# Performance work log

Measured on AMD Instinct MI355X. Metric: run time of the kernel, lower is better.

## Reference

```python
import jax, jax.numpy as jnp
import numpy as np

B, E, H, NH, HD = 8, 1536, 256, 8, 32
L, V, NL, FF = 50, 50257, 4, 2048
BOS = 50256
EPS = 1e-5


def setup_inputs():
    key = jax.random.key(0)
    ks = jax.random.split(key, 12)
    s = 0.02

    def rn(k, shape):
        return jax.random.normal(k, shape, jnp.float32) * s

    return {
        "embedding": jax.random.normal(ks[0], (B, E), jnp.float32),
        "w_proj": rn(ks[1], (H, E)), "b_proj": jnp.zeros((H,), jnp.float32),
        "tok_emb": rn(ks[2], (V, H)),
        "pos_enc": rn(ks[3], (1, L, H)),
        "sa_in_w": rn(ks[4], (NL, 3 * H, H)), "sa_in_b": jnp.zeros((NL, 3 * H), jnp.float32),
        "sa_out_w": rn(ks[5], (NL, H, H)), "sa_out_b": jnp.zeros((NL, H), jnp.float32),
        "ca_in_w": rn(ks[6], (NL, 3 * H, H)), "ca_in_b": jnp.zeros((NL, 3 * H), jnp.float32),
        "ca_out_w": rn(ks[7], (NL, H, H)), "ca_out_b": jnp.zeros((NL, H), jnp.float32),
        "ff1_w": rn(ks[8], (NL, FF, H)), "ff1_b": jnp.zeros((NL, FF), jnp.float32),
        "ff2_w": rn(ks[9], (NL, H, FF)), "ff2_b": jnp.zeros((NL, H), jnp.float32),
        "ln_g": jnp.ones((NL, 3, H), jnp.float32), "ln_b": jnp.zeros((NL, 3, H), jnp.float32),
        "fc_w": rn(ks[10], (V, H)), "fc_b": jnp.zeros((V,), jnp.float32),
    }


def _ln(x, g, b):
    m = jnp.mean(x, -1, keepdims=True)
    v = jnp.mean((x - m) ** 2, -1, keepdims=True)
    return (x - m) * jax.lax.rsqrt(v + EPS) * g + b


def _mha(q_in, kv_in, in_w, in_b, out_w, out_b, mask):
    wq, wk, wv = jnp.split(in_w, 3, axis=0)
    bq, bk, bv = jnp.split(in_b, 3)

    def heads(t):
        b_, l_, _ = t.shape
        return t.reshape(b_, l_, NH, HD).transpose(0, 2, 1, 3)  # [B,NH,L,HD]

    q = heads(q_in @ wq.T + bq)
    k = heads(kv_in @ wk.T + bk)
    v = heads(kv_in @ wv.T + bv)
    scores = jnp.einsum('bhqd,bhkd->bhqk', q, k) * (1.0 / np.sqrt(HD))
    if mask is not None:
        scores = scores + mask
    a = jax.nn.softmax(scores, axis=-1)
    o = jnp.einsum('bhqk,bhkd->bhqd', a, v)
    o = o.transpose(0, 2, 1, 3).reshape(q_in.shape)
    return o @ out_w.T + out_b


def _decoder(x, mem, mask, p):
    # nn.TransformerDecoderLayer, post-LN, relu FFN
    for l in range(NL):
        x = _ln(x + _mha(x, x, p['sa_in_w'][l], p['sa_in_b'][l], p['sa_out_w'][l], p['sa_out_b'][l], mask), p['ln_g'][l, 0], p['ln_b'][l, 0])
        x = _ln(x + _mha(x, mem, p['ca_in_w'][l], p['ca_in_b'][l], p['ca_out_w'][l], p['ca_out_b'][l], None), p['ln_g'][l, 1], p['ln_b'][l, 1])
        h = jax.nn.relu(x @ p['ff1_w'][l].T + p['ff1_b'][l]) @ p['ff2_w'][l].T + p['ff2_b'][l]
        x = _ln(x + h, p['ln_g'][l, 2], p['ln_b'][l, 2])
    return x


def _forward(embedding, tok_emb, pos_enc, w_proj, b_proj, fc_w, fc_b, p):
    mem = (embedding @ w_proj.T + b_proj)[:, None, :]  # [B,1,H] single-token memory
    causal = jnp.tril(jnp.ones((L, L), bool))
    mask = jnp.where(causal, 0.0, -jnp.inf)[None, None]  # [1,1,L,L]
    tokens0 = jnp.full((B, L), BOS, jnp.int32)  # padded token buffer; pos 0 = BOS

    # At step t the original recomputes the decoder over the first t+1 tokens and
    # reads the last position. With a causal mask, position t of a full-length
    # decode depends only on tokens[:t+1], so decoding the padded buffer and
    # slicing position t is exactly the same math (no-KV-cache recompute kept).
    def step(tokens, t):
        x = tok_emb[tokens] + pos_enc[:, :L]
        x = _decoder(x, mem, mask, p)
        h_t = jax.lax.dynamic_slice_in_dim(x, t, 1, axis=1)[:, 0]  # [B,H]
        logits = h_t @ fc_w.T + fc_b  # [B,V]
        nxt = jnp.argmax(logits, -1).astype(jnp.int32)
        tokens = jax.lax.dynamic_update_slice_in_dim(tokens, nxt[:, None], t + 1, axis=1)
        return tokens, logits

    _, logits = jax.lax.scan(step, tokens0, jnp.arange(L - 1))
    return jnp.transpose(logits, (1, 0, 2))  # [B, L-1, V]


def reference(embedding, w_proj, b_proj, tok_emb, pos_enc, sa_in_w, sa_in_b, sa_out_w, sa_out_b, ca_in_w, ca_in_b, ca_out_w, ca_out_b, ff1_w, ff1_b, ff2_w, ff2_b, ln_g, ln_b, fc_w, fc_b):
    p = dict(sa_in_w=sa_in_w, sa_in_b=sa_in_b, sa_out_w=sa_out_w, sa_out_b=sa_out_b,
             ca_in_w=ca_in_w, ca_in_b=ca_in_b, ca_out_w=ca_out_w, ca_out_b=ca_out_b,
             ff1_w=ff1_w, ff1_b=ff1_b, ff2_w=ff2_w, ff2_b=ff2_b, ln_g=ln_g, ln_b=ln_b)
    return _forward(embedding, tok_emb, pos_enc, w_proj, b_proj, fc_w, fc_b, p)
```

## Files before the change

### kernel.cpp

```cpp
#include <hip/hip_runtime.h>

#define NV 50257
#define BOSTOK 50256
#define LNEPS 1e-5f
#define NSTEP 49
#define NBLK 256
#define RPB 197
#define DYN_LDS_BYTES ((256 * 52 + 50 * 256) * 4)
#define FSTR 64

#define FQKV(l)   (0 + (l))
#define FU(l)     (4 + (l))
#define FFPX(l,j) (8 + (l) * 8 + (j))
#define FFC(j)    (48 + (j))
#define FMEMF     56
#define FCAF      57

#define WS4_MEM 4096
#define WS4_CA  6144
#define WS4_XF  14336
#define WS4_Q   16384
#define WS4_K   18432
#define WS4_V   20480
#define WS4_U   22528
#define WS4_FFP 30720
#define WS4_PV  63488
#define WS4_PI  65536

__device__ __forceinline__ float gld(const float* p) {
  return __hip_atomic_load(const_cast<float*>(p), __ATOMIC_RELAXED, __HIP_MEMORY_SCOPE_AGENT);
}
__device__ __forceinline__ void gst(float* p, float v) {
  __hip_atomic_store(p, v, __ATOMIC_RELAXED, __HIP_MEMORY_SCOPE_AGENT);
}
__device__ __forceinline__ void gsti(int* p, int v) {
  __hip_atomic_store(p, v, __ATOMIC_RELAXED, __HIP_MEMORY_SCOPE_AGENT);
}
__device__ __forceinline__ unsigned fld(unsigned* p) {
  return __hip_atomic_load(p, __ATOMIC_RELAXED, __HIP_MEMORY_SCOPE_AGENT);
}
__device__ __forceinline__ void spin_burst(float z) {
#pragma unroll
  for (int i = 0; i < 64; ++i) z = __builtin_fmaf(z, 1.0000001f, 1e-30f);
  asm volatile("" :: "v"(z));
}
__device__ __forceinline__ void bump(unsigned* f) {
  asm volatile("s_waitcnt vmcnt(0)" ::: "memory");
  __syncthreads();
  if (threadIdx.x == 0)
    __hip_atomic_fetch_add(f, 1u, __ATOMIC_RELAXED, __HIP_MEMORY_SCOPE_AGENT);
}
__device__ __forceinline__ void bump8(unsigned* f) {
  asm volatile("s_waitcnt vmcnt(0)" ::: "memory");
  __syncthreads();
  if (threadIdx.x == 0)
    for (int j = 0; j < 8; ++j)
      __hip_atomic_fetch_add(f + j * FSTR, 1u, __ATOMIC_RELAXED, __HIP_MEMORY_SCOPE_AGENT);
}
__device__ __forceinline__ unsigned waitf(unsigned* f, unsigned tgt, unsigned* sh) {
  if (threadIdx.x == 0) {
    unsigned v = fld(f);
    while (v < tgt) { spin_burst((float)v); v = fld(f); }
    *sh = v;
  }
  __syncthreads();
  return *sh;
}
__device__ __forceinline__ unsigned wait_fcsum(unsigned* FL, unsigned tgt, unsigned* sh) {
  if (threadIdx.x == 0) {
    const unsigned* bp = FL + 48 * FSTR;
    unsigned s;
    for (;;) {
      unsigned a0, a1, a2, a3, a4, a5, a6, a7;
      asm volatile(
          "global_load_dword %0, %8, off sc0 sc1\n\t"
          "global_load_dword %1, %8, off offset:256 sc0 sc1\n\t"
          "global_load_dword %2, %8, off offset:512 sc0 sc1\n\t"
          "global_load_dword %3, %8, off offset:768 sc0 sc1\n\t"
          "global_load_dword %4, %8, off offset:1024 sc0 sc1\n\t"
          "global_load_dword %5, %8, off offset:1280 sc0 sc1\n\t"
          "global_load_dword %6, %8, off offset:1536 sc0 sc1\n\t"
          "global_load_dword %7, %8, off offset:1792 sc0 sc1\n\t"
          "s_waitcnt vmcnt(0)"
          : "=&v"(a0), "=&v"(a1), "=&v"(a2), "=&v"(a3),
            "=&v"(a4), "=&v"(a5), "=&v"(a6), "=&v"(a7)
          : "v"(bp) : "memory");
      s = a0 + a1 + a2 + a3 + a4 + a5 + a6 + a7;
      if (s >= tgt) break;
      spin_burst((float)s);
    }
    *sh = s;
  }
  __syncthreads();
  return *sh;
}

__device__ __forceinline__ void pull2p(float* x, float* y,
    const float* p0, const float* p1, unsigned salt) {
  asm("global_load_dword %0, %2, off sc0 sc1\n\t"
      "global_load_dword %1, %3, off sc0 sc1\n\t"
      "s_waitcnt vmcnt(0)"
      : "=&v"(*x), "=&v"(*y)
      : "v"(p0), "v"(p1), "v"(salt));
}
__device__ __forceinline__ void pull3p(float* x, float* y, float* z,
    const float* p0, const float* p1, const float* p2, unsigned salt) {
  asm("global_load_dword %0, %3, off sc0 sc1\n\t"
      "global_load_dword %1, %4, off sc0 sc1\n\t"
      "global_load_dword %2, %5, off sc0 sc1\n\t"
      "s_waitcnt vmcnt(0)"
      : "=&v"(*x), "=&v"(*y), "=&v"(*z)
      : "v"(p0), "v"(p1), "v"(p2), "v"(salt));
}
__device__ __forceinline__ void pull8p(float r[8],
    const float* p0, const float* p1, const float* p2, const float* p3,
    const float* p4, const float* p5, const float* p6, const float* p7, unsigned salt) {
  float a0, a1, a2, a3, a4, a5, a6, a7;
  asm("global_load_dword %0, %8, off sc0 sc1\n\t"
      "global_load_dword %1, %9, off sc0 sc1\n\t"
      "global_load_dword %2, %10, off sc0 sc1\n\t"
      "global_load_dword %3, %11, off sc0 sc1\n\t"
      "global_load_dword %4, %12, off sc0 sc1\n\t"
      "global_load_dword %5, %13, off sc0 sc1\n\t"
      "global_load_dword %6, %14, off sc0 sc1\n\t"
      "global_load_dword %7, %15, off sc0 sc1\n\t"
      "s_waitcnt vmcnt(0)"
      : "=&v"(a0), "=&v"(a1), "=&v"(a2), "=&v"(a3),
        "=&v"(a4), "=&v"(a5), "=&v"(a6), "=&v"(a7)
      : "v"(p0), "v"(p1), "v"(p2), "v"(p3), "v"(p4), "v"(p5), "v"(p6), "v"(p7), "v"(salt));
  r[0] = a0; r[1] = a1; r[2] = a2; r[3] = a3;
  r[4] = a4; r[5] = a5; r[6] = a6; r[7] = a7;
}
__device__ __forceinline__ void pull1_2q(float* u, float4* f0, float4* f1,
    const float* pu, const float* pf, unsigned salt) {
  asm("global_load_dword %0, %3, off sc0 sc1\n\t"
      "global_load_dwordx4 %1, %4, off sc0 sc1\n\t"
      "global_load_dwordx4 %2, %4, off offset:16 sc0 sc1\n\t"
      "s_waitcnt vmcnt(0)"
      : "=&v"(*u), "=&v"(*f0), "=&v"(*f1)
      : "v"(pu), "v"(pf), "v"(salt));
}
__device__ __forceinline__ void pull4x8(float4 r[8],
    const float* p0, const float* p1, const float* p2, const float* p3, unsigned salt) {
  float4 a0, a1, a2, a3, a4, a5, a6, a7;
  asm("global_load_dwordx4 %0, %8, off sc0 sc1\n\t"
      "global_load_dwordx4 %1, %8, off offset:16 sc0 sc1\n\t"
      "global_load_dwordx4 %2, %9, off sc0 sc1\n\t"
      "global_load_dwordx4 %3, %9, off offset:16 sc0 sc1\n\t"
      "global_load_dwordx4 %4, %10, off sc0 sc1\n\t"
      "global_load_dwordx4 %5, %10, off offset:16 sc0 sc1\n\t"
      "global_load_dwordx4 %6, %11, off sc0 sc1\n\t"
      "global_load_dwordx4 %7, %11, off offset:16 sc0 sc1\n\t"
      "s_waitcnt vmcnt(0)"
      : "=&v"(a0), "=&v"(a1), "=&v"(a2), "=&v"(a3),
        "=&v"(a4), "=&v"(a5), "=&v"(a6), "=&v"(a7)
      : "v"(p0), "v"(p1), "v"(p2), "v"(p3), "v"(salt));
  r[0] = a0; r[1] = a1; r[2] = a2; r[3] = a3;
  r[4] = a4; r[5] = a5; r[6] = a6; r[7] = a7;
}

__device__ __forceinline__ float block_ln256(float v, int tid, float* red8, float g, float bta) {
  float s = v, s2 = v * v;
#pragma unroll
  for (int m = 32; m >= 1; m >>= 1) { s += __shfl_xor(s, m); s2 += __shfl_xor(s2, m); }
  int w = tid >> 6;
  __syncthreads();
  if ((tid & 63) == 0) { red8[w] = s; red8[4 + w] = s2; }
  __syncthreads();
  s = red8[0] + red8[1] + red8[2] + red8[3];
  s2 = red8[4] + red8[5] + red8[6] + red8[7];
  float mn = s * (1.0f / 256.0f);
  float var = s2 * (1.0f / 256.0f) - mn * mn;
  float rs = rsqrtf(var + LNEPS);
  return (v - mn) * rs * g + bta;
}

__device__ __forceinline__ void finalln_fc(int bid, int tid, int t, unsigned salt,
                                           const float* u, const float* ffp,
                                           const float* ff2_b, const float* ln_g,
                                           const float* ln_b,
                                           const float* fc_w, const float* fc_b, float* out,
                                           float* pv, int* pi,
                                           float* xl, float* rv, int* ri, float* red8) {
  {
    float u8[8];
    pull8p(u8, u + 3 * 2048 + 0 * 256 + tid, u + 3 * 2048 + 1 * 256 + tid,
           u + 3 * 2048 + 2 * 256 + tid, u + 3 * 2048 + 3 * 256 + tid,
           u + 3 * 2048 + 4 * 256 + tid, u + 3 * 2048 + 5 * 256 + tid,
           u + 3 * 2048 + 6 * 256 + tid, u + 3 * 2048 + 7 * 256 + tid, salt);
    float4 fA[8], fB[8];
    const float* fb = ffp + 1 * 16384;
    pull4x8(fA, fb + (0 * 256 + tid) * 8, fb + (1 * 256 + tid) * 8,
            fb + (2 * 256 + tid) * 8, fb + (3 * 256 + tid) * 8, salt);
    pull4x8(fB, fb + (4 * 256 + tid) * 8, fb + (5 * 256 + tid) * 8,
            fb + (6 * 256 + tid) * 8, fb + (7 * 256 + tid) * 8, salt);
    float g = ln_g[(3 * 3 + 2) * 256 + tid], bt = ln_b[(3 * 3 + 2) * 256 + tid];
    float f2b = ff2_b[3 * 256 + tid];
#pragma unroll
    for (int b = 0; b < 8; ++b) {
      float4 q0 = (b < 4) ? fA[2 * b] : fB[2 * (b - 4)];
      float4 q1 = (b < 4) ? fA[2 * b + 1] : fB[2 * (b - 4) + 1];
      float a = u8[b] + f2b + q0.x + q0.y + q0.z + q0.w + q1.x + q1.y + q1.z + q1.w;
      xl[b * 260 + tid] = block_ln256(a, tid, red8, g, bt);
    }
  }
  __syncthreads();
  int r = tid >> 3, b = tid & 7;
  float bv = -3e38f; int bi = 2147483647;
  int base = bid * RPB;
  for (int i = 0; i < 7; ++i) {
    int rr = i * 32 + r, row = base + rr;
    if (rr < RPB && row < NV) {
      float acc = fc_b[row];
      const float4* w4 = reinterpret_cast<const float4*>(fc_w + (size_t)row * 256);
      const float4* xv = reinterpret_cast<const float4*>(xl + b * 260);
      for (int k = 0; k < 64; ++k) {
        float4 wv = w4[k]; float4 xq = xv[k];
        acc += wv.x * xq.x + wv.y * xq.y + wv.z * xq.z + wv.w * xq.w;
      }
      out[(size_t)(b * 49 + t) * NV + row] = acc;
      if (acc > bv || (acc == bv && row < bi)) { bv = acc; bi = row; }
    }
  }
  rv[tid] = bv; ri[tid] = bi;
  __syncthreads();
  for (int off = 128; off >= 8; off >>= 1) {
    if (tid < off) {
      float v = rv[tid + off]; int id = ri[tid + off];
      if (v > rv[tid] || (v == rv[tid] && id < ri[tid])) { rv[tid] = v; ri[tid] = id; }
    }
    __syncthreads();
  }
  if (tid < 8) { gst(pv + bid * 8 + tid, rv[tid]); gsti(pi + bid * 8 + tid, ri[tid]); }
}

__global__ __launch_bounds__(256) void k_flow6(
    const float* __restrict__ emb, const float* __restrict__ w_proj, const float* __restrict__ b_proj,
    const float* __restrict__ tok_emb, const float* __restrict__ pos_enc,
    const float* __restrict__ sa_in_w, const float* __restrict__ sa_in_b,
    const float* __restrict__ sa_out_w, const float* __restrict__ sa_out_b,
    const float* __restrict__ ca_in_w, const float* __restrict__ ca_in_b,
    const float* __restrict__ ca_out_w, const float* __restrict__ ca_out_b,
    const float* __restrict__ ff1_w, const float* __restrict__ ff1_b,
    const float* __restrict__ ff2_w, const float* __restrict__ ff2_b,
    const float* __restrict__ ln_g, const float* __restrict__ ln_b,
    const float* __restrict__ fc_w, const float* __restrict__ fc_b,
    float* __restrict__ out, float* __restrict__ wsf, int* __restrict__ wsi) {
  extern __shared__ float dynlds[];
  const int bid = blockIdx.x, tid = threadIdx.x;

  unsigned* FL = (unsigned*)wsf;
  float* mem = wsf + WS4_MEM;
  float* ca  = wsf + WS4_CA;
  float* qb  = wsf + WS4_Q;
  float* kb  = wsf + WS4_K;
  float* vb  = wsf + WS4_V;
  float* u   = wsf + WS4_U;
  float* ffp = wsf + WS4_FFP;
  float* pv  = wsf + WS4_PV;
  int*   pi  = wsi + WS4_PI;

  __shared__ float xl[8 * 260];
  __shared__ float h1l[256 * 9];
  __shared__ float ql[256], ol[256], ph[8 * 64];
  __shared__ float red8[8];
  __shared__ float rv[256];
  __shared__ int   ri[256];
  __shared__ int   toks[8];
  __shared__ unsigned saltsh;
  __shared__ float el[1536];

  if (bid < 64) {
    int b = bid >> 3, tile = bid & 7;
    for (int k = tid; k < 1536; k += 256) el[k] = emb[b * 1536 + k];
    __syncthreads();
    int r = tid >> 3, g = tid & 7;
    int row = tile * 32 + r;
    float acc = 0.f;
    const float* wr = w_proj + (size_t)row * 1536;
    for (int c = g * 192; c < g * 192 + 192; ++c) acc += wr[c] * el[c];
    rv[tid] = acc;
    __syncthreads();
    for (int off = 4; off >= 1; off >>= 1) {
      if (g < off) rv[tid] += rv[tid + off];
      __syncthreads();
    }
    if (g == 0) gst(mem + b * 256 + row, rv[tid] + b_proj[row]);
    bump(FL + FMEMF * FSTR);
  }
  if (bid >= 64 && bid < 96) {
    unsigned s0 = waitf(FL + FMEMF * FSTR, 64u, &saltsh);
    int l = (bid - 64) >> 3, b = (bid - 64) & 7;
    ql[tid] = gld(mem + b * 256 + tid) + 0.f * (float)(s0 & 0);
    __syncthreads();
    float acc = ca_in_b[l * 768 + 512 + tid];
    const float* wr = ca_in_w + (size_t)(l * 768 + 512 + tid) * 256;
    for (int c = 0; c < 256; ++c) acc += wr[c] * ql[c];
    ol[tid] = acc;
    __syncthreads();
    float acc2 = ca_out_b[l * 256 + tid];
    const float* wr2 = ca_out_w + (size_t)(l * 256 + tid) * 256;
    for (int c = 0; c < 256; ++c) acc2 += wr2[c] * ol[c];
    gst(ca + (l * 8 + b) * 256 + tid, acc2);
    bump(FL + FCAF * FSTR);
  }

  if (bid < 32) {
    int myl = bid >> 3, myb = bid & 7;
    float* Klds = dynlds;
    float* Vlds = dynlds + 256 * 52;
    unsigned sc = waitf(FL + FCAF * FSTR, 32u, &saltsh);
    float caval = gld(ca + ((myl * 8 + myb) * 256 + (int)(sc & 0)) + tid);
    for (int t = 0; t < NSTEP; ++t) {
      float xres;
      if (myl == 0) {
        if (t > 0) {
          unsigned s = wait_fcsum(FL, 256u * (unsigned)t, &saltsh);
          float pvv, piv;
          pull2p(&pvv, &piv, pv + tid * 8 + myb, (const float*)(pi + tid * 8 + myb), s);
          rv[tid] = pvv; ri[tid] = __float_as_int(piv);
          __syncthreads();
          for (int off = 128; off >= 1; off >>= 1) {
            if (tid < off) {
              float v = rv[tid + off]; int id = ri[tid + off];
              if (v > rv[tid] || (v == rv[tid] && id < ri[tid])) { rv[tid] = v; ri[tid] = id; }
            }
            __syncthreads();
          }
          if (tid == 0) toks[0] = ri[0];
          __syncthreads();
        } else {
          if (tid == 0) toks[0] = BOSTOK;
          __syncthreads();
        }
        xres = tok_emb[(size_t)toks[0] * 256 + tid] + pos_enc[t * 256 + tid];
      } else {
        unsigned s = waitf(FL + FFPX(myl - 1, bid & 7) * FSTR, 8u * (unsigned)(t + 1), &saltsh);
        float uv; float4 f0, f1;
        int par = (myl - 1) & 1;
        pull1_2q(&uv, &f0, &f1, u + (myl - 1) * 2048 + myb * 256 + tid,
                 ffp + par * 16384 + (myb * 256 + tid) * 8, s);
        float a = uv + ff2_b[(myl - 1) * 256 + tid]
                + f0.x + f0.y + f0.z + f0.w + f1.x + f1.y + f1.z + f1.w;
        xres = block_ln256(a, tid, red8, ln_g[((myl - 1) * 3 + 2) * 256 + tid],
                           ln_b[((myl - 1) * 3 + 2) * 256 + tid]);
      }
      unsigned s2 = waitf(FL + FQKV(myl) * FSTR, 24u * (unsigned)(t + 1), &saltsh);
      float qv, kv, vv;
      pull3p(&qv, &kv, &vv, qb + myb * 256 + tid, kb + myb * 256 + tid, vb + myb * 256 + tid, s2);
      ql[tid] = qv;
      Klds[tid * 52 + t] = kv;
      Vlds[t * 256 + tid] = vv;
      __syncthreads();
      int h = tid >> 5, j0 = tid & 31;
      const float* qh = ql + h * 32;
      float s0v = -3e38f, s1v = -3e38f;
      if (j0 <= t) {
        float d0 = 0.f;
#pragma unroll
        for (int d = 0; d < 32; ++d) d0 += qh[d] * Klds[(h * 32 + d) * 52 + j0];
        s0v = d0 * 0.17677669529663687f;
      }
      if (j0 + 32 <= t) {
        float d1 = 0.f;
#pragma unroll
        for (int d = 0; d < 32; ++d) d1 += qh[d] * Klds[(h * 32 + d) * 52 + j0 + 32];
        s1v = d1 * 0.17677669529663687f;
      }
      float mx = fmaxf(s0v, s1v);
      for (int m = 16; m >= 1; m >>= 1) mx = fmaxf(mx, __shfl_xor(mx, m, 32));
      float e0 = (j0 <= t) ? expf(s0v - mx) : 0.f;
      float e1 = (j0 + 32 <= t) ? expf(s1v - mx) : 0.f;
      float sm = e0 + e1;
      for (int m = 16; m >= 1; m >>= 1) sm += __shfl_xor(sm, m, 32);
      ph[h * 64 + j0] = e0;
      ph[h * 64 + j0 + 32] = e1;
      __syncthreads();
      float o = 0.f;
      for (int j = 0; j <= t; ++j) o += ph[h * 64 + j] * Vlds[j * 256 + tid];
      ol[tid] = o / sm;
      __syncthreads();
      float acc = sa_out_b[myl * 256 + tid];
      const float4* w4 = reinterpret_cast<const float4*>(sa_out_w + (size_t)(myl * 256 + tid) * 256);
#pragma unroll 4
      for (int k = 0; k < 64; ++k) {
        float4 wv = w4[k];
        acc += wv.x * ol[4 * k] + wv.y * ol[4 * k + 1] + wv.z * ol[4 * k + 2] + wv.w * ol[4 * k + 3];
      }
      acc += xres;
      float y = block_ln256(acc, tid, red8, ln_g[(myl * 3 + 0) * 256 + tid],
                            ln_b[(myl * 3 + 0) * 256 + tid]);
      float y2 = block_ln256(y + caval, tid, red8,
                             ln_g[(myl * 3 + 1) * 256 + tid], ln_b[(myl * 3 + 1) * 256 + tid]);
      gst(u + myl * 2048 + myb * 256 + tid, y2);
      bump(FL + FU(myl) * FSTR);

      unsigned s4 = waitf(FL + FFPX(3, bid & 7) * FSTR, 8u * (unsigned)(t + 1), &saltsh);
      finalln_fc(bid, tid, t, s4, u, ffp, ff2_b, ln_g, ln_b, fc_w, fc_b, out, pv, pi,
                 xl, rv, ri, red8);
      bump(FL + FFC(bid & 7) * FSTR);
    }
  } else if (bid < 56) {
    int qi = bid - 32;
    for (int t = 0; t < NSTEP; ++t) {
      for (int l = 0; l < 4; ++l) {
        if (l == 0) {
          if (t == 0) {
            if (tid < 8) toks[tid] = BOSTOK;
            __syncthreads();
          } else {
            unsigned s = wait_fcsum(FL, 256u * (unsigned)t, &saltsh);
            int i0 = tid >> 3, b = tid & 7;
            float pvv[8], piv[8];
            pull8p(pvv, pv + (i0 + 0) * 8 + b, pv + (i0 + 32) * 8 + b, pv + (i0 + 64) * 8 + b,
                   pv + (i0 + 96) * 8 + b, pv + (i0 + 128) * 8 + b, pv + (i0 + 160) * 8 + b,
                   pv + (i0 + 192) * 8 + b, pv + (i0 + 224) * 8 + b, s);
            const float* pif = (const float*)pi;
            pull8p(piv, pif + (i0 + 0) * 8 + b, pif + (i0 + 32) * 8 + b, pif + (i0 + 64) * 8 + b,
                   pif + (i0 + 96) * 8 + b, pif + (i0 + 128) * 8 + b, pif + (i0 + 160) * 8 + b,
                   pif + (i0 + 192) * 8 + b, pif + (i0 + 224) * 8 + b, s);
            float bv = -3e38f; int bi = 2147483647;
#pragma unroll
            for (int k = 0; k < 8; ++k) {
              float v = pvv[k]; int id = __float_as_int(piv[k]);
              if (v > bv || (v == bv && id < bi)) { bv = v; bi = id; }
            }
            rv[tid] = bv; ri[tid] = bi;
            __syncthreads();
            for (int off = 128; off >= 8; off >>= 1) {
              if (tid < off) {
                float v = rv[tid + off]; int id = ri[tid + off];
                if (v > rv[tid] || (v == rv[tid] && id < ri[tid])) { rv[tid] = v; ri[tid] = id; }
              }
              __syncthreads();
            }
            if (tid < 8) toks[tid] = ri[tid];
            __syncthreads();
          }
          for (int b = 0; b < 8; ++b)
            xl[b * 260 + tid] = tok_emb[(size_t)toks[b] * 256 + tid] + pos_enc[t * 256 + tid];
          __syncthreads();
        } else {
          unsigned s = waitf(FL + FFPX(l - 1, bid & 7) * FSTR, 8u * (unsigned)(t + 1), &saltsh);
          int lp = l - 1, par = lp & 1;
          float u8[8];
          pull8p(u8, u + lp * 2048 + 0 * 256 + tid, u + lp * 2048 + 1 * 256 + tid,
                 u + lp * 2048 + 2 * 256 + tid, u + lp * 2048 + 3 * 256 + tid,
                 u + lp * 2048 + 4 * 256 + tid, u + lp * 2048 + 5 * 256 + tid,
                 u + lp * 2048 + 6 * 256 + tid, u + lp * 2048 + 7 * 256 + tid, s);
          float4 fA[8], fB[8];
          const float* fb = ffp + par * 16384;
          pull4x8(fA, fb + (0 * 256 + tid) * 8, fb + (1 * 256 + tid) * 8,
                  fb + (2 * 256 + tid) * 8, fb + (3 * 256 + tid) * 8, s);
          pull4x8(fB, fb + (4 * 256 + tid) * 8, fb + (5 * 256 + tid) * 8,
                  fb + (6 * 256 + tid) * 8, fb + (7 * 256 + tid) * 8, s);
          float g = ln_g[(lp * 3 + 2) * 256 + tid], bt = ln_b[(lp * 3 + 2) * 256 + tid];
          float f2b = ff2_b[lp * 256 + tid];
#pragma unroll
          for (int b = 0; b < 8; ++b) {
            float4 q0 = (b < 4) ? fA[2 * b] : fB[2 * (b - 4)];
            float4 q1 = (b < 4) ? fA[2 * b + 1] : fB[2 * (b - 4) + 1];
            float a = u8[b] + f2b + q0.x + q0.y + q0.z + q0.w + q1.x + q1.y + q1.z + q1.w;
            xl[b * 260 + tid] = block_ln256(a, tid, red8, g, bt);
          }
          __syncthreads();
        }
        int r = tid >> 3, b8 = tid & 7;
        int row = qi * 32 + r;
        float acc = sa_in_b[l * 768 + row];
        const float4* w4 = reinterpret_cast<const float4*>(sa_in_w + (size_t)(l * 768 + row) * 256);
        const float4* xv = reinterpret_cast<const float4*>(xl + b8 * 260);
#pragma unroll 8
        for (int k = 0; k < 64; ++k) {
          float4 wv = w4[k]; float4 xq = xv[k];
          acc += wv.x * xq.x + wv.y * xq.y + wv.z * xq.z + wv.w * xq.w;
        }
        if (row < 256) gst(qb + b8 * 256 + row, acc);
        else if (row < 512) gst(kb + b8 * 256 + (row - 256), acc);
        else gst(vb + b8 * 256 + (row - 512), acc);
        bump(FL + FQKV(l) * FSTR);
      }
      unsigned s4 = waitf(FL + FFPX(3, bid & 7) * FSTR, 8u * (unsigned)(t + 1), &saltsh);
      finalln_fc(bid, tid, t, s4, u, ffp, ff2_b, ln_g, ln_b, fc_w, fc_b, out, pv, pi,
                 xl, rv, ri, red8);
      bump(FL + FFC(bid & 7) * FSTR);
    }
  } else if (bid < 64) {
    int s = bid - 56;
    for (int t = 0; t < NSTEP; ++t) {
      for (int l = 0; l < 4; ++l) {
        unsigned sv = waitf(FL + FU(l) * FSTR, 8u * (unsigned)(t + 1), &saltsh);
        {
          float u8[8];
          pull8p(u8, u + l * 2048 + 0 * 256 + tid, u + l * 2048 + 1 * 256 + tid,
                 u + l * 2048 + 2 * 256 + tid, u + l * 2048 + 3 * 256 + tid,
                 u + l * 2048 + 4 * 256 + tid, u + l * 2048 + 5 * 256 + tid,
                 u + l * 2048 + 6 * 256 + tid, u + l * 2048 + 7 * 256 + tid, sv);
#pragma unroll
          for (int b = 0; b < 8; ++b) xl[b * 260 + tid] = u8[b];
        }
        __syncthreads();
        {
          int row = s * 256 + tid;
          float acc[8];
          float bb = ff1_b[l * 2048 + row];
#pragma unroll
          for (int b = 0; b < 8; ++b) acc[b] = bb;
          const float4* w4 = reinterpret_cast<const float4*>(ff1_w + (size_t)(l * 2048 + row) * 256);
          for (int k = 0; k < 64; ++k) {
            float4 wv = w4[k];
#pragma unroll
            for (int b = 0; b < 8; ++b) {
              const float4 xq = reinterpret_cast<const float4*>(xl + b * 260)[k];
              acc[b] += wv.x * xq.x + wv.y * xq.y + wv.z * xq.z + wv.w * xq.w;
            }
          }
#pragma unroll
          for (int b = 0; b < 8; ++b) h1l[tid * 9 + b] = fmaxf(acc[b], 0.f);
        }
        __syncthreads();
        {
          float facc[8] = {0, 0, 0, 0, 0, 0, 0, 0};
          const float* w2p = ff2_w + (size_t)(l * 256 + tid) * 2048 + s * 256;
          for (int n = 0; n < 256; ++n) {
            float wv = w2p[n];
#pragma unroll
            for (int b = 0; b < 8; ++b) facc[b] += wv * h1l[n * 9 + b];
          }
          int par = l & 1;
#pragma unroll
          for (int b = 0; b < 8; ++b)
            gst(ffp + par * 16384 + (b * 256 + tid) * 8 + s, facc[b]);
        }
        bump8(FL + FFPX(l, 0) * FSTR);
        __syncthreads();
      }
      unsigned s4 = waitf(FL + FFPX(3, bid & 7) * FSTR, 8u * (unsigned)(t + 1), &saltsh);
      finalln_fc(bid, tid, t, s4, u, ffp, ff2_b, ln_g, ln_b, fc_w, fc_b, out, pv, pi,
                 xl, rv, ri, red8);
      bump(FL + FFC(bid & 7) * FSTR);
    }
  } else {
    for (int t = 0; t < NSTEP; ++t) {
      unsigned s4 = waitf(FL + FFPX(3, bid & 7) * FSTR, 8u * (unsigned)(t + 1), &saltsh);
      finalln_fc(bid, tid, t, s4, u, ffp, ff2_b, ln_g, ln_b, fc_w, fc_b, out, pv, pi,
                 xl, rv, ri, red8);
      bump(FL + FFC(bid & 7) * FSTR);
    }
  }
}

extern "C" void kernel_launch(void* const* d_in, const int* in_sizes, int n_in,
                              void* d_out, int out_size, void* d_ws, size_t ws_size,
                              hipStream_t stream) {
  (void)in_sizes; (void)n_in; (void)out_size; (void)ws_size;
  const float* embedding = (const float*)d_in[0];
  const float* w_proj   = (const float*)d_in[1];
  const float* b_proj   = (const float*)d_in[2];
  const float* tok_emb  = (const float*)d_in[3];
  const float* pos_enc  = (const float*)d_in[4];
  const float* sa_in_w  = (const float*)d_in[5];
  const float* sa_in_b  = (const float*)d_in[6];
  const float* sa_out_w = (const float*)d_in[7];
  const float* sa_out_b = (const float*)d_in[8];
  const float* ca_in_w  = (const float*)d_in[9];
  const float* ca_in_b  = (const float*)d_in[10];
  const float* ca_out_w = (const float*)d_in[11];
  const float* ca_out_b = (const float*)d_in[12];
  const float* ff1_w    = (const float*)d_in[13];
  const float* ff1_b    = (const float*)d_in[14];
  const float* ff2_w    = (const float*)d_in[15];
  const float* ff2_b    = (const float*)d_in[16];
  const float* ln_g     = (const float*)d_in[17];
  const float* ln_b     = (const float*)d_in[18];
  const float* fc_w     = (const float*)d_in[19];
  const float* fc_b     = (const float*)d_in[20];
  float* out = (float*)d_out;
  float* wsf = (float*)d_ws;
  int*   wsi = (int*)d_ws;

  (void)hipFuncSetAttribute(reinterpret_cast<const void*>(k_flow6),
                            hipFuncAttributeMaxDynamicSharedMemorySize, DYN_LDS_BYTES);
  (void)hipMemsetAsync(d_ws, 0, 16384, stream);
  hipLaunchKernelGGL(k_flow6, dim3(NBLK), dim3(256), DYN_LDS_BYTES, stream,
                     embedding, w_proj, b_proj, tok_emb, pos_enc,
                     sa_in_w, sa_in_b, sa_out_w, sa_out_b,
                     ca_in_w, ca_in_b, ca_out_w, ca_out_b,
                     ff1_w, ff1_b, ff2_w, ff2_b,
                     ln_g, ln_b, fc_w, fc_b,
                     out, wsf, wsi);
}
```

Before: 10.75 ms.

## Compute QKV projection locally per attention block, drop dedicated QKV producer blocks

After: 13.01 ms. 21.0% more time.

```diff
diff --git a/kernel.cpp b/kernel.cpp
--- a/kernel.cpp
+++ b/kernel.cpp
@@ -9,7 +9,6 @@
 #define DYN_LDS_BYTES ((256 * 52 + 50 * 256) * 4)
 #define FSTR 64
 
-#define FQKV(l)   (0 + (l))
 #define FU(l)     (4 + (l))
 #define FFPX(l,j) (8 + (l) * 8 + (j))
 #define FFC(j)    (48 + (j))
@@ -18,10 +17,6 @@
 
 #define WS4_MEM 4096
 #define WS4_CA  6144
-#define WS4_XF  14336
-#define WS4_Q   16384
-#define WS4_K   18432
-#define WS4_V   20480
 #define WS4_U   22528
 #define WS4_FFP 30720
 #define WS4_PV  63488
@@ -39,11 +34,6 @@
 __device__ __forceinline__ unsigned fld(unsigned* p) {
   return __hip_atomic_load(p, __ATOMIC_RELAXED, __HIP_MEMORY_SCOPE_AGENT);
 }
-__device__ __forceinline__ void spin_burst(float z) {
-#pragma unroll
-  for (int i = 0; i < 64; ++i) z = __builtin_fmaf(z, 1.0000001f, 1e-30f);
-  asm volatile("" :: "v"(z));
-}
 __device__ __forceinline__ void bump(unsigned* f) {
   asm volatile("s_waitcnt vmcnt(0)" ::: "memory");
   __syncthreads();
@@ -60,7 +50,7 @@
 __device__ __forceinline__ unsigned waitf(unsigned* f, unsigned tgt, unsigned* sh) {
   if (threadIdx.x == 0) {
     unsigned v = fld(f);
-    while (v < tgt) { spin_burst((float)v); v = fld(f); }
+    while (v < tgt) { __builtin_amdgcn_s_sleep(1); v = fld(f); }
     *sh = v;
   }
   __syncthreads();
@@ -69,7 +59,6 @@
 __device__ __forceinline__ unsigned wait_fcsum(unsigned* FL, unsigned tgt, unsigned* sh) {
   if (threadIdx.x == 0) {
     const unsigned* bp = FL + 48 * FSTR;
-    unsigned s;
     for (;;) {
       unsigned a0, a1, a2, a3, a4, a5, a6, a7;
       asm volatile(
@@ -85,11 +74,10 @@
           : "=&v"(a0), "=&v"(a1), "=&v"(a2), "=&v"(a3),
             "=&v"(a4), "=&v"(a5), "=&v"(a6), "=&v"(a7)
           : "v"(bp) : "memory");
-      s = a0 + a1 + a2 + a3 + a4 + a5 + a6 + a7;
-      if (s >= tgt) break;
-      spin_burst((float)s);
-    }
-    *sh = s;
+      unsigned s = a0 + a1 + a2 + a3 + a4 + a5 + a6 + a7;
+      if (s >= tgt) { *sh = s; break; }
+      __builtin_amdgcn_s_sleep(1);
+    }
   }
   __syncthreads();
   return *sh;
@@ -102,15 +90,6 @@
       "s_waitcnt vmcnt(0)"
       : "=&v"(*x), "=&v"(*y)
       : "v"(p0), "v"(p1), "v"(salt));
-}
-__device__ __forceinline__ void pull3p(float* x, float* y, float* z,
-    const float* p0, const float* p1, const float* p2, unsigned salt) {
-  asm("global_load_dword %0, %3, off sc0 sc1\n\t"
-      "global_load_dword %1, %4, off sc0 sc1\n\t"
-      "global_load_dword %2, %5, off sc0 sc1\n\t"
-      "s_waitcnt vmcnt(0)"
-      : "=&v"(*x), "=&v"(*y), "=&v"(*z)
-      : "v"(p0), "v"(p1), "v"(p2), "v"(salt));
 }
 __device__ __forceinline__ void pull8p(float r[8],
     const float* p0, const float* p1, const float* p2, const float* p3,
@@ -218,7 +197,7 @@
         float4 wv = w4[k]; float4 xq = xv[k];
         acc += wv.x * xq.x + wv.y * xq.y + wv.z * xq.z + wv.w * xq.w;
       }
-      out[(size_t)(b * 49 + t) * NV + row] = acc;
+      __builtin_nontemporal_store(acc, &out[(size_t)(b * 49 + t) * NV + row]);
       if (acc > bv || (acc == bv && row < bi)) { bv = acc; bi = row; }
     }
   }
@@ -234,7 +213,7 @@
   if (tid < 8) { gst(pv + bid * 8 + tid, rv[tid]); gsti(pi + bid * 8 + tid, ri[tid]); }
 }
 
-__global__ __launch_bounds__(256) void k_flow6(
+__global__ __launch_bounds__(256) void k_flow8(
     const float* __restrict__ emb, const float* __restrict__ w_proj, const float* __restrict__ b_proj,
     const float* __restrict__ tok_emb, const float* __restrict__ pos_enc,
     const float* __restrict__ sa_in_w, const float* __restrict__ sa_in_b,
@@ -252,15 +231,13 @@
   unsigned* FL = (unsigned*)wsf;
   float* mem = wsf + WS4_MEM;
   float* ca  = wsf + WS4_CA;
-  float* qb  = wsf + WS4_Q;
-  float* kb  = wsf + WS4_K;
-  float* vb  = wsf + WS4_V;
   float* u   = wsf + WS4_U;
   float* ffp = wsf + WS4_FFP;
   float* pv  = wsf + WS4_PV;
   int*   pi  = wsi + WS4_PI;
 
   __shared__ float xl[8 * 260];
+  __shared__ float xrow[256];
   __shared__ float h1l[256 * 9];
   __shared__ float ql[256], ol[256], ph[8 * 64];
   __shared__ float red8[8];
@@ -345,9 +322,27 @@
         xres = block_ln256(a, tid, red8, ln_g[((myl - 1) * 3 + 2) * 256 + tid],
                            ln_b[((myl - 1) * 3 + 2) * 256 + tid]);
       }
-      unsigned s2 = waitf(FL + FQKV(myl) * FSTR, 24u * (unsigned)(t + 1), &saltsh);
+      xrow[tid] = xres;
+      __syncthreads();
       float qv, kv, vv;
-      pull3p(&qv, &kv, &vv, qb + myb * 256 + tid, kb + myb * 256 + tid, vb + myb * 256 + tid, s2);
+      {
+        const float4* xq4 = reinterpret_cast<const float4*>(xrow);
+#pragma unroll
+        for (int rr = 0; rr < 3; ++rr) {
+          int row = tid + rr * 256;
+          float acc = sa_in_b[myl * 768 + row];
+          const float4* w4 = reinterpret_cast<const float4*>(sa_in_w + (size_t)(myl * 768 + row) * 256);
+#pragma unroll 8
+          for (int k = 0; k < 64; ++k) {
+            float4 wv = w4[k]; float4 xq = xq4[k];
+            acc += wv.x * xq.x + wv.y * xq.y + wv.z * xq.z + wv.w * xq.w;
+          }
+          if (rr == 0) qv = acc;
+          else if (rr == 1) kv = acc;
+          else vv = acc;
+        }
+      }
+      __syncthreads();
       ql[tid] = qv;
       Klds[tid * 52 + t] = kv;
       Vlds[t * 256 + tid] = vv;
@@ -400,92 +395,7 @@
                  xl, rv, ri, red8);
       bump(FL + FFC(bid & 7) * FSTR);
     }
-  } else if (bid < 56) {
-    int qi = bid - 32;
-    for (int t = 0; t < NSTEP; ++t) {
-      for (int l = 0; l < 4; ++l) {
-        if (l == 0) {
-          if (t == 0) {
-            if (tid < 8) toks[tid] = BOSTOK;
-            __syncthreads();
-          } else {
-            unsigned s = wait_fcsum(FL, 256u * (unsigned)t, &saltsh);
-            int i0 = tid >> 3, b = tid & 7;
-            float pvv[8], piv[8];
-            pull8p(pvv, pv + (i0 + 0) * 8 + b, pv + (i0 + 32) * 8 + b, pv + (i0 + 64) * 8 + b,
-                   pv + (i0 + 96) * 8 + b, pv + (i0 + 128) * 8 + b, pv + (i0 + 160) * 8 + b,
-                   pv + (i0 + 192) * 8 + b, pv + (i0 + 224) * 8 + b, s);
-            const float* pif = (const float*)pi;
-            pull8p(piv, pif + (i0 + 0) * 8 + b, pif + (i0 + 32) * 8 + b, pif + (i0 + 64) * 8 + b,
-                   pif + (i0 + 96) * 8 + b, pif + (i0 + 128) * 8 + b, pif + (i0 + 160) * 8 + b,
-                   pif + (i0 + 192) * 8 + b, pif + (i0 + 224) * 8 + b, s);
-            float bv = -3e38f; int bi = 2147483647;
-#pragma unroll
-            for (int k = 0; k < 8; ++k) {
-              float v = pvv[k]; int id = __float_as_int(piv[k]);
-              if (v > bv || (v == bv && id < bi)) { bv = v; bi = id; }
-            }
-            rv[tid] = bv; ri[tid] = bi;
-            __syncthreads();
-            for (int off = 128; off >= 8; off >>= 1) {
-              if (tid < off) {
-                float v = rv[tid + off]; int id = ri[tid + off];
-                if (v > rv[tid] || (v == rv[tid] && id < ri[tid])) { rv[tid] = v; ri[tid] = id; }
-              }
-              __syncthreads();
-            }
-            if (tid < 8) toks[tid] = ri[tid];
-            __syncthreads();
-          }
-          for (int b = 0; b < 8; ++b)
-            xl[b * 260 + tid] = tok_emb[(size_t)toks[b] * 256 + tid] + pos_enc[t * 256 + tid];
-          __syncthreads();
-        } else {
-          unsigned s = waitf(FL + FFPX(l - 1, bid & 7) * FSTR, 8u * (unsigned)(t + 1), &saltsh);
-          int lp = l - 1, par = lp & 1;
-          float u8[8];
-          pull8p(u8, u + lp * 2048 + 0 * 256 + tid, u + lp * 2048 + 1 * 256 + tid,
-                 u + lp * 2048 + 2 * 256 + tid, u + lp * 2048 + 3 * 256 + tid,
-                 u + lp * 2048 + 4 * 256 + tid, u + lp * 2048 + 5 * 256 + tid,
-                 u + lp * 2048 + 6 * 256 + tid, u + lp * 2048 + 7 * 256 + tid, s);
-          float4 fA[8], fB[8];
-          const float* fb = ffp + par * 16384;
-          pull4x8(fA, fb + (0 * 256 + tid) * 8, fb + (1 * 256 + tid) * 8,
-                  fb + (2 * 256 + tid) * 8, fb + (3 * 256 + tid) * 8, s);
-          pull4x8(fB, fb + (4 * 256 + tid) * 8, fb + (5 * 256 + tid) * 8,
-                  fb + (6 * 256 + tid) * 8, fb + (7 * 256 + tid) * 8, s);
-          float g = ln_g[(lp * 3 + 2) * 256 + tid], bt = ln_b[(lp * 3 + 2) * 256 + tid];
-          float f2b = ff2_b[lp * 256 + tid];
-#pragma unroll
-          for (int b = 0; b < 8; ++b) {
-            float4 q0 = (b < 4) ? fA[2 * b] : fB[2 * (b - 4)];
-            float4 q1 = (b < 4) ? fA[2 * b + 1] : fB[2 * (b - 4) + 1];
-            float a = u8[b] + f2b + q0.x + q0.y + q0.z + q0.w + q1.x + q1.y + q1.z + q1.w;
-            xl[b * 260 + tid] = block_ln256(a, tid, red8, g, bt);
-          }
-          __syncthreads();
-        }
-        int r = tid >> 3, b8 = tid & 7;
-        int row = qi * 32 + r;
-        float acc = sa_in_b[l * 768 + row];
-        const float4* w4 = reinterpret_cast<const float4*>(sa_in_w + (size_t)(l * 768 + row) * 256);
-        const float4* xv = reinterpret_cast<const float4*>(xl + b8 * 260);
-#pragma unroll 8
-        for (int k = 0; k < 64; ++k) {
-          float4 wv = w4[k]; float4 xq = xv[k];
-          acc += wv.x * xq.x + wv.y * xq.y + wv.z * xq.z + wv.w * xq.w;
-        }
-        if (row < 256) gst(qb + b8 * 256 + row, acc);
-        else if (row < 512) gst(kb + b8 * 256 + (row - 256), acc);
-        else gst(vb + b8 * 256 + (row - 512), acc);
-        bump(FL + FQKV(l) * FSTR);
-      }
-      unsigned s4 = waitf(FL + FFPX(3, bid & 7) * FSTR, 8u * (unsigned)(t + 1), &saltsh);
-      finalln_fc(bid, tid, t, s4, u, ffp, ff2_b, ln_g, ln_b, fc_w, fc_b, out, pv, pi,
-                 xl, rv, ri, red8);
-      bump(FL + FFC(bid & 7) * FSTR);
-    }
-  } else if (bid < 64) {
+  } else if (bid >= 56 && bid < 64) {
     int s = bid - 56;
     for (int t = 0; t < NSTEP; ++t) {
       for (int l = 0; l < 4; ++l) {
@@ -579,10 +489,10 @@
   float* wsf = (float*)d_ws;
   int*   wsi = (int*)d_ws;
 
-  (void)hipFuncSetAttribute(reinterpret_cast<const void*>(k_flow6),
+  (void)hipFuncSetAttribute(reinterpret_cast<const void*>(k_flow8),
                             hipFuncAttributeMaxDynamicSharedMemorySize, DYN_LDS_BYTES);
   (void)hipMemsetAsync(d_ws, 0, 16384, stream);
-  hipLaunchKernelGGL(k_flow6, dim3(NBLK), dim3(256), DYN_LDS_BYTES, stream,
+  hipLaunchKernelGGL(k_flow8, dim3(NBLK), dim3(256), DYN_LDS_BYTES, stream,
                      embedding, w_proj, b_proj, tok_emb, pos_enc,
                      sa_in_w, sa_in_b, sa_out_w, sa_out_b,
                      ca_in_w, ca_in_b, ca_out_w, ca_out_b,
```
